# Kernel optimization log

Hardware: AMD Instinct MI355X
Metric: run time of the kernel (lower is better)

The kernel has to match this reference:

```python
import jax, jax.numpy as jnp
import numpy as np

B, N, IN_DIM, OUT_DIM, H = 8, 1024, 256, 256, 4
HD = OUT_DIM // H  # head_dim = 64
NEG = -1e9
EPS = 1e-5


def setup_inputs() -> dict:
    key = jax.random.key(0)
    ks = jax.random.split(key, 9)
    h = jax.random.normal(ks[0], (B, N, IN_DIM), dtype=jnp.float32)
    adj = jax.random.randint(ks[1], (N, N), 0, 2, dtype=jnp.int32)
    adj = adj.at[jnp.arange(N), jnp.arange(N)].set(1)  # self loops so no empty rows
    s = 1.0 / np.sqrt(IN_DIM)
    W = jax.random.uniform(ks[2], (H, IN_DIM, HD), jnp.float32, -s, s)
    sa = 1.0 / np.sqrt(2 * HD)
    a1 = jax.random.uniform(ks[3], (H, HD), jnp.float32, -sa, sa)
    a2 = jax.random.uniform(ks[4], (H, HD), jnp.float32, -sa, sa)
    sp = 1.0 / np.sqrt(OUT_DIM)
    proj_w = jax.random.uniform(ks[5], (OUT_DIM, OUT_DIM), jnp.float32, -sp, sp)
    proj_b = jax.random.uniform(ks[6], (OUT_DIM,), jnp.float32, -sp, sp)
    gamma = jnp.ones((OUT_DIM,), jnp.float32)
    beta = jnp.zeros((OUT_DIM,), jnp.float32)
    return {"h": h, "adj": adj, "W": W, "a1": a1, "a2": a2,
            "proj_w": proj_w, "proj_b": proj_b, "gamma": gamma, "beta": beta}


def reference(h, adj, W, a1, a2, proj_w, proj_b, gamma, beta):
    # Wh: [B,H,N,HD]
    Wh = jnp.einsum('bni,hid->bhnd', h, W)
    # Decompose a([Wh_i || Wh_j]) = a1.Wh_i + a2.Wh_j (same math as concat+linear)
    si = jnp.einsum('bhnd,hd->bhn', Wh, a1)  # [B,H,N]
    sj = jnp.einsum('bhnd,hd->bhn', Wh, a2)
    e = jax.nn.leaky_relu(si[:, :, :, None] + sj[:, :, None, :], 0.2)  # [B,H,N,N]
    mask = (adj == 0)  # [N,N]
    e = jnp.where(mask[None, None], NEG, e)
    alpha = jax.nn.softmax(e, axis=-1)
    out = jnp.einsum('bhnm,bhmd->bhnd', alpha, Wh)  # [B,H,N,HD]
    h_multi = out.transpose(0, 2, 1, 3).reshape(B, N, OUT_DIM)  # concat heads
    h_out = jnp.einsum('bnd,od->bno', h_multi, proj_w) + proj_b
    h_out = h_out + h  # residual (in_dim == out_dim)
    mu = jnp.mean(h_out, axis=-1, keepdims=True)
    var = jnp.mean(jnp.square(h_out - mu), axis=-1, keepdims=True)
    return (h_out - mu) * jax.lax.rsqrt(var + EPS) * gamma + beta
```

## Files before the change

### kernel.cpp

```cpp
#include <hip/hip_runtime.h>
#include <hip/hip_bf16.h>

#define BB 8
#define NN 1024
#define IN_DIM 256
#define OUT_DIM 256
#define NH 4
#define HD 64
#define TN 16
#define PSTRIDE 1032

typedef __attribute__((ext_vector_type(8))) short short8;
typedef __attribute__((ext_vector_type(4))) short short4e;
typedef __attribute__((ext_vector_type(4))) float floatx4;
typedef __attribute__((ext_vector_type(4))) int intx4;

__global__ __launch_bounds__(256) void prep_kernel(
    const float* __restrict__ W,
    const float* __restrict__ a1, const float* __restrict__ a2,
    const float* __restrict__ proj_w,
    __hip_bfloat16* __restrict__ WTb,
    __hip_bfloat16* __restrict__ pwb,
    __hip_bfloat16* __restrict__ wab)
{
    int blk = blockIdx.x, t = threadIdx.x;
    if (blk < 16) {
        int o = blk * 16 + (t >> 4);
        int hh = o >> 6, d = o & 63;
        #pragma unroll
        for (int kk = 0; kk < 16; ++kk) {
            int k = (t & 15) + 16 * kk;
            WTb[(size_t)o * 256 + k] = __float2bfloat16(W[((size_t)hh * 256 + k) * 64 + d]);
        }
    } else if (blk < 32) {
        size_t base = (size_t)(blk - 16) * 4096 + t * 16;
        #pragma unroll
        for (int k = 0; k < 16; k += 4) {
            floatx4 v = *(const floatx4*)(proj_w + base + k);
            alignas(8) __hip_bfloat16 tmp[4];
            #pragma unroll
            for (int j = 0; j < 4; ++j) tmp[j] = __float2bfloat16(v[j]);
            *(short4e*)(pwb + base + k) = *(const short4e*)tmp;
        }
    } else {
        int r = blk - 32;
        int hh = r & 3;
        const float* av = (r < 4 ? a1 : a2) + hh * HD;
        const float* wrow = W + ((size_t)hh * 256 + t) * HD;
        float s = 0.f;
        #pragma unroll 8
        for (int d = 0; d < HD; ++d) s += wrow[d] * av[d];
        wab[(size_t)r * 256 + t] = __float2bfloat16(s);
        wab[(size_t)(r + 8) * 256 + t] = __float2bfloat16(0.f);
    }
}

__global__ __launch_bounds__(256) void wh_mfma_kernel(
    const float* __restrict__ h,
    const __hip_bfloat16* __restrict__ WTb,
    const __hip_bfloat16* __restrict__ wab,
    __hip_bfloat16* __restrict__ WhT,
    float* __restrict__ si, float* __restrict__ sj)
{
    int t = threadIdx.x;
    int w = t >> 6, l = t & 63;
    int rl = l & 15, q = l >> 4;
    int r0 = blockIdx.x * 16;

    short8 af[8];
    const float* Arow = h + (size_t)(r0 + rl) * 256 + q * 8;
    #pragma unroll
    for (int k0 = 0; k0 < 8; ++k0) {
        floatx4 v0 = *(const floatx4*)(Arow + k0 * 32);
        floatx4 v1 = *(const floatx4*)(Arow + k0 * 32 + 4);
        short8 a;
        #pragma unroll
        for (int j = 0; j < 4; ++j) {
            a[j]     = (short)(__bfloat16_as_ushort(__float2bfloat16(v0[j])));
            a[j + 4] = (short)(__bfloat16_as_ushort(__float2bfloat16(v1[j])));
        }
        af[k0] = a;
    }

    int bb = r0 >> 10;
    int n0 = (r0 & 1023) + q * 4;

    #pragma unroll
    for (int j = 0; j < 4; ++j) {
        int ct = w + j * 4;
        const __hip_bfloat16* Brow = WTb + (size_t)(ct * 16 + rl) * 256 + q * 8;
        floatx4 acc = {0.f, 0.f, 0.f, 0.f};
        #pragma unroll
        for (int k0 = 0; k0 < 8; ++k0) {
            short8 bf = *(const short8*)(Brow + k0 * 32);
            acc = __builtin_amdgcn_mfma_f32_16x16x32_bf16(af[k0], bf, acc, 0, 0, 0);
        }
        int o = ct * 16 + rl;
        int hh = o >> 6, d = o & 63;
        alignas(8) __hip_bfloat16 tmp[4];
        #pragma unroll
        for (int i = 0; i < 4; ++i) tmp[i] = __float2bfloat16(acc[i]);
        *(short4e*)(WhT + ((size_t)(bb * NH + hh) * HD + d) * NN + n0) = *(const short4e*)tmp;
    }

    if (w == 0) {
        const __hip_bfloat16* Brow = wab + (size_t)rl * 256 + q * 8;
        floatx4 acc = {0.f, 0.f, 0.f, 0.f};
        #pragma unroll
        for (int k0 = 0; k0 < 8; ++k0) {
            short8 bf = *(const short8*)(Brow + k0 * 32);
            acc = __builtin_amdgcn_mfma_f32_16x16x32_bf16(af[k0], bf, acc, 0, 0, 0);
        }
        if (rl < 8) {
            int hh = rl & 3;
            float* dst = (rl < 4 ? si : sj) + ((size_t)(bb * NH + hh)) * NN + n0;
            *(floatx4*)dst = acc;
        }
    }
}

__global__ __launch_bounds__(256) void attn_kernel(
    const int* __restrict__ adj,
    const __hip_bfloat16* __restrict__ WhT,
    const float* __restrict__ si,
    const float* __restrict__ sj,
    __hip_bfloat16* __restrict__ hmb)
{
    int bx = blockIdx.x;
    int bh = bx >> 6;
    int n0 = (bx & 63) * TN;
    int t = threadIdx.x;

    __shared__ __align__(16) __hip_bfloat16 p_lds[TN * PSTRIDE];
    __shared__ float rinv[TN];

    int r = t >> 4;
    int c = t & 15;
    int n = n0 + r;
    float sii = si[(size_t)bh * NN + n];
    const float* sjr = sj + (size_t)bh * NN;
    const int* adjr = adj + (size_t)n * NN;

    float lsum = 0.f;
    #pragma unroll 4
    for (int jj = 0; jj < 16; ++jj) {
        int m = jj * 64 + c * 4;
        floatx4 s4 = *(const floatx4*)(sjr + m);
        intx4 a4 = *(const intx4*)(adjr + m);
        alignas(8) __hip_bfloat16 tmp[4];
        #pragma unroll
        for (int k = 0; k < 4; ++k) {
            float x = sii + s4[k];
            x = x > 0.f ? x : 0.2f * x;
            x = (a4[k] == 0) ? -1e9f : x;
            float pv = __expf(x);
            lsum += pv;
            tmp[k] = __float2bfloat16(pv);
        }
        *(short4e*)(p_lds + (size_t)r * PSTRIDE + m) = *(const short4e*)tmp;
    }
    #pragma unroll
    for (int off = 1; off < 16; off <<= 1) lsum += __shfl_xor(lsum, off, 64);
    if (c == 0) rinv[r] = 1.f / lsum;
    __syncthreads();

    int w = t >> 6;
    int l = t & 63;
    int rl = l & 15, q = l >> 4;
    int d0 = w * 16;
    const __hip_bfloat16* Bbase = WhT + ((size_t)bh * HD + d0 + rl) * NN + q * 8;
    const __hip_bfloat16* Abase = p_lds + (size_t)rl * PSTRIDE + q * 8;

    floatx4 acc = {0.f, 0.f, 0.f, 0.f};
    #pragma unroll 4
    for (int k0 = 0; k0 < NN; k0 += 32) {
        short8 af = *(const short8*)(Abase + k0);
        short8 bf = *(const short8*)(Bbase + k0);
        acc = __builtin_amdgcn_mfma_f32_16x16x32_bf16(af, bf, acc, 0, 0, 0);
    }

    int b = bh >> 2, hhh = bh & 3;
    #pragma unroll
    for (int i = 0; i < 4; ++i) {
        int nr = q * 4 + i;
        float v = acc[i] * rinv[nr];
        hmb[((size_t)(b * NN) + n0 + nr) * OUT_DIM + hhh * HD + d0 + rl] = __float2bfloat16(v);
    }
}

__global__ __launch_bounds__(256) void proj_ln_kernel(
    const __hip_bfloat16* __restrict__ hmb,
    const float* __restrict__ h,
    const __hip_bfloat16* __restrict__ pwb,
    const float* __restrict__ proj_b,
    const float* __restrict__ gamma,
    const float* __restrict__ beta,
    float* __restrict__ out)
{
    int t = threadIdx.x;
    int w = t >> 6, l = t & 63;
    int rl = l & 15, q = l >> 4;
    int r0 = blockIdx.x * 16;

    __shared__ float red[2][4][16];

    short8 af[8];
    const __hip_bfloat16* Arow = hmb + (size_t)(r0 + rl) * 256 + q * 8;
    #pragma unroll
    for (int k0 = 0; k0 < 8; ++k0) af[k0] = *(const short8*)(Arow + k0 * 32);

    floatx4 acc[4];
    #pragma unroll
    for (int j = 0; j < 4; ++j) {
        int ct = w + j * 4;
        const __hip_bfloat16* Brow = pwb + (size_t)(ct * 16 + rl) * 256 + q * 8;
        floatx4 a = {0.f, 0.f, 0.f, 0.f};
        #pragma unroll
        for (int k0 = 0; k0 < 8; ++k0) {
            short8 bf = *(const short8*)(Brow + k0 * 32);
            a = __builtin_amdgcn_mfma_f32_16x16x32_bf16(af[k0], bf, a, 0, 0, 0);
        }
        acc[j] = a;
    }

    float ps[4] = {0.f, 0.f, 0.f, 0.f};
    #pragma unroll
    for (int j = 0; j < 4; ++j) {
        int col = (w + j * 4) * 16 + rl;
        float pb = proj_b[col];
        #pragma unroll
        for (int i = 0; i < 4; ++i) {
            float v = acc[j][i] + pb + h[(size_t)(r0 + q * 4 + i) * 256 + col];
            acc[j][i] = v;
            ps[i] += v;
        }
    }
    #pragma unroll
    for (int i = 0; i < 4; ++i) {
        float s = ps[i];
        #pragma unroll
        for (int off = 1; off < 16; off <<= 1) s += __shfl_xor(s, off, 64);
        ps[i] = s;
    }
    if (rl == 0) {
        for (int i = 0; i < 4; ++i) red[0][w][q * 4 + i] = ps[i];
    }
    __syncthreads();
    float mu[4];
    #pragma unroll
    for (int i = 0; i < 4; ++i) {
        int row = q * 4 + i;
        mu[i] = (red[0][0][row] + red[0][1][row] + red[0][2][row] + red[0][3][row]) * (1.f / 256.f);
    }

    float vs[4] = {0.f, 0.f, 0.f, 0.f};
    #pragma unroll
    for (int j = 0; j < 4; ++j) {
        #pragma unroll
        for (int i = 0; i < 4; ++i) { float cv = acc[j][i] - mu[i]; vs[i] += cv * cv; }
    }
    #pragma unroll
    for (int i = 0; i < 4; ++i) {
        float s = vs[i];
        #pragma unroll
        for (int off = 1; off < 16; off <<= 1) s += __shfl_xor(s, off, 64);
        vs[i] = s;
    }
    if (rl == 0) {
        for (int i = 0; i < 4; ++i) red[1][w][q * 4 + i] = vs[i];
    }
    __syncthreads();
    float rs[4];
    #pragma unroll
    for (int i = 0; i < 4; ++i) {
        int row = q * 4 + i;
        float var = (red[1][0][row] + red[1][1][row] + red[1][2][row] + red[1][3][row]) * (1.f / 256.f);
        rs[i] = rsqrtf(var + 1e-5f);
    }

    #pragma unroll
    for (int j = 0; j < 4; ++j) {
        int col = (w + j * 4) * 16 + rl;
        float g = gamma[col], be = beta[col];
        #pragma unroll
        for (int i = 0; i < 4; ++i)
            out[(size_t)(r0 + q * 4 + i) * 256 + col] = (acc[j][i] - mu[i]) * rs[i] * g + be;
    }
}

extern "C" void kernel_launch(void* const* d_in, const int* in_sizes, int n_in,
                              void* d_out, int out_size, void* d_ws, size_t ws_size,
                              hipStream_t stream) {
    const float* h      = (const float*)d_in[0];
    const int*   adj    = (const int*)d_in[1];
    const float* W      = (const float*)d_in[2];
    const float* a1     = (const float*)d_in[3];
    const float* a2     = (const float*)d_in[4];
    const float* proj_w = (const float*)d_in[5];
    const float* proj_b = (const float*)d_in[6];
    const float* gamma  = (const float*)d_in[7];
    const float* beta   = (const float*)d_in[8];
    float* out = (float*)d_out;

    char* ws = (char*)d_ws;
    __hip_bfloat16* WhT = (__hip_bfloat16*)ws;                    ws += (size_t)BB*NH*HD*NN*2;
    __hip_bfloat16* hmb = (__hip_bfloat16*)ws;                    ws += (size_t)BB*NN*OUT_DIM*2;
    __hip_bfloat16* WTb = (__hip_bfloat16*)ws;                    ws += 256*256*2;
    __hip_bfloat16* pwb = (__hip_bfloat16*)ws;                    ws += 256*256*2;
    __hip_bfloat16* wab = (__hip_bfloat16*)ws;                    ws += 16*256*2;
    float* si = (float*)ws;                                       ws += (size_t)BB*NH*NN*4;
    float* sj = (float*)ws;

    prep_kernel<<<40, 256, 0, stream>>>(W, a1, a2, proj_w, WTb, pwb, wab);
    wh_mfma_kernel<<<512, 256, 0, stream>>>(h, WTb, wab, WhT, si, sj);
    attn_kernel<<<BB * NH * (NN / TN), 256, 0, stream>>>(adj, WhT, si, sj, hmb);
    proj_ln_kernel<<<512, 256, 0, stream>>>(hmb, h, pwb, proj_b, gamma, beta, out);
}
```

Before: 144.7 us.

## Fuse all four GAT stages into one cooperative kernel with grid syncs

Replaces the four separate launches (prep, Wh GEMM, attention, projection+LayerNorm) with a single cooperative kernel of 512 blocks that separates the stages with grid-wide syncs. Each block processes four attention tiles in a loop. The aim is to remove launch overhead and inter-kernel gaps. In exchange it adds grid barrier cost, and occupancy is limited because every block now reserves the attention stage's ~33KB LDS buffer even during the GEMM phases. The cooperative launch also needs all 512 blocks to be co-resident.

```diff
diff --git a/kernel.cpp b/kernel.cpp
--- a/kernel.cpp
+++ b/kernel.cpp
@@ -1,5 +1,8 @@
 #include <hip/hip_runtime.h>
 #include <hip/hip_bf16.h>
+#include <hip/hip_cooperative_groups.h>
+
+namespace cg = cooperative_groups;
 
 #define BB 8
 #define NN 1024
@@ -15,15 +18,28 @@
 typedef __attribute__((ext_vector_type(4))) float floatx4;
 typedef __attribute__((ext_vector_type(4))) int intx4;
 
-__global__ __launch_bounds__(256) void prep_kernel(
-    const float* __restrict__ W,
-    const float* __restrict__ a1, const float* __restrict__ a2,
-    const float* __restrict__ proj_w,
+__global__ __launch_bounds__(256) void fused_gat_kernel(
+    const float* __restrict__ h, const int* __restrict__ adj,
+    const float* __restrict__ W, const float* __restrict__ a1, const float* __restrict__ a2,
+    const float* __restrict__ proj_w, const float* __restrict__ proj_b,
+    const float* __restrict__ gamma, const float* __restrict__ beta,
+    float* __restrict__ out,
     __hip_bfloat16* __restrict__ WTb,
     __hip_bfloat16* __restrict__ pwb,
-    __hip_bfloat16* __restrict__ wab)
+    __hip_bfloat16* __restrict__ wab,
+    __hip_bfloat16* __restrict__ WhT,
+    float* __restrict__ si, float* __restrict__ sj,
+    __hip_bfloat16* __restrict__ hmb)
 {
+    cg::grid_group grid = cg::this_grid();
     int blk = blockIdx.x, t = threadIdx.x;
+    int w = t >> 6, l = t & 63;
+    int rl = l & 15, q = l >> 4;
+
+    __shared__ __align__(16) __hip_bfloat16 p_lds[TN * PSTRIDE];
+    __shared__ float rinv[TN];
+    __shared__ float red[2][4][16];
+
     if (blk < 16) {
         int o = blk * 16 + (t >> 4);
         int hh = o >> 6, d = o & 63;
@@ -42,7 +58,7 @@
             for (int j = 0; j < 4; ++j) tmp[j] = __float2bfloat16(v[j]);
             *(short4e*)(pwb + base + k) = *(const short4e*)tmp;
         }
-    } else {
+    } else if (blk < 40) {
         int r = blk - 32;
         int hh = r & 3;
         const float* av = (r < 4 ? a1 : a2) + hh * HD;
@@ -53,238 +69,209 @@
         wab[(size_t)r * 256 + t] = __float2bfloat16(s);
         wab[(size_t)(r + 8) * 256 + t] = __float2bfloat16(0.f);
     }
-}
-
-__global__ __launch_bounds__(256) void wh_mfma_kernel(
-    const float* __restrict__ h,
-    const __hip_bfloat16* __restrict__ WTb,
-    const __hip_bfloat16* __restrict__ wab,
-    __hip_bfloat16* __restrict__ WhT,
-    float* __restrict__ si, float* __restrict__ sj)
-{
-    int t = threadIdx.x;
-    int w = t >> 6, l = t & 63;
-    int rl = l & 15, q = l >> 4;
-    int r0 = blockIdx.x * 16;
-
-    short8 af[8];
-    const float* Arow = h + (size_t)(r0 + rl) * 256 + q * 8;
-    #pragma unroll
-    for (int k0 = 0; k0 < 8; ++k0) {
-        floatx4 v0 = *(const floatx4*)(Arow + k0 * 32);
-        floatx4 v1 = *(const floatx4*)(Arow + k0 * 32 + 4);
-        short8 a;
-        #pragma unroll
-        for (int j = 0; j < 4; ++j) {
-            a[j]     = (short)(__bfloat16_as_ushort(__float2bfloat16(v0[j])));
-            a[j + 4] = (short)(__bfloat16_as_ushort(__float2bfloat16(v1[j])));
-        }
-        af[k0] = a;
+    __threadfence();
+    grid.sync();
+
+    {
+        int r0 = blk * 16;
+        short8 af[8];
+        const float* Arow = h + (size_t)(r0 + rl) * 256 + q * 8;
+        #pragma unroll
+        for (int k0 = 0; k0 < 8; ++k0) {
+            floatx4 v0 = *(const floatx4*)(Arow + k0 * 32);
+            floatx4 v1 = *(const floatx4*)(Arow + k0 * 32 + 4);
+            short8 a;
+            #pragma unroll
+            for (int j = 0; j < 4; ++j) {
+                a[j]     = (short)(__bfloat16_as_ushort(__float2bfloat16(v0[j])));
+                a[j + 4] = (short)(__bfloat16_as_ushort(__float2bfloat16(v1[j])));
+            }
+            af[k0] = a;
+        }
+
+        int bb = r0 >> 10;
+        int n0 = (r0 & 1023) + q * 4;
+
+        #pragma unroll
+        for (int j = 0; j < 4; ++j) {
+            int ct = w + j * 4;
+            const __hip_bfloat16* Brow = WTb + (size_t)(ct * 16 + rl) * 256 + q * 8;
+            floatx4 acc = {0.f, 0.f, 0.f, 0.f};
+            #pragma unroll
+            for (int k0 = 0; k0 < 8; ++k0) {
+                short8 bf = *(const short8*)(Brow + k0 * 32);
+                acc = __builtin_amdgcn_mfma_f32_16x16x32_bf16(af[k0], bf, acc, 0, 0, 0);
+            }
+            int o = ct * 16 + rl;
+            int hh = o >> 6, d = o & 63;
+            alignas(8) __hip_bfloat16 tmp[4];
+            #pragma unroll
+            for (int i = 0; i < 4; ++i) tmp[i] = __float2bfloat16(acc[i]);
+            *(short4e*)(WhT + ((size_t)(bb * NH + hh) * HD + d) * NN + n0) = *(const short4e*)tmp;
+        }
+
+        if (w == 0) {
+            const __hip_bfloat16* Brow = wab + (size_t)rl * 256 + q * 8;
+            floatx4 acc = {0.f, 0.f, 0.f, 0.f};
+            #pragma unroll
+            for (int k0 = 0; k0 < 8; ++k0) {
+                short8 bf = *(const short8*)(Brow + k0 * 32);
+                acc = __builtin_amdgcn_mfma_f32_16x16x32_bf16(af[k0], bf, acc, 0, 0, 0);
+            }
+            if (rl < 8) {
+                int hh = rl & 3;
+                float* dst = (rl < 4 ? si : sj) + ((size_t)(bb * NH + hh)) * NN + n0;
+                *(floatx4*)dst = acc;
+            }
+        }
     }
-
-    int bb = r0 >> 10;
-    int n0 = (r0 & 1023) + q * 4;
-
-    #pragma unroll
-    for (int j = 0; j < 4; ++j) {
-        int ct = w + j * 4;
-        const __hip_bfloat16* Brow = WTb + (size_t)(ct * 16 + rl) * 256 + q * 8;
+    __threadfence();
+    grid.sync();
+
+    for (int it = 0; it < 4; ++it) {
+        __syncthreads();
+        int bx = blk * 4 + it;
+        int bh = bx >> 6;
+        int n0 = (bx & 63) * TN;
+
+        int r = t >> 4;
+        int c = t & 15;
+        int n = n0 + r;
+        float sii = si[(size_t)bh * NN + n];
+        const float* sjr = sj + (size_t)bh * NN;
+        const int* adjr = adj + (size_t)n * NN;
+
+        float lsum = 0.f;
+        #pragma unroll 4
+        for (int jj = 0; jj < 16; ++jj) {
+            int m = jj * 64 + c * 4;
+            floatx4 s4 = *(const floatx4*)(sjr + m);
+            intx4 a4 = *(const intx4*)(adjr + m);
+            alignas(8) __hip_bfloat16 tmp[4];
+            #pragma unroll
+            for (int k = 0; k < 4; ++k) {
+                float x = sii + s4[k];
+                x = x > 0.f ? x : 0.2f * x;
+                x = (a4[k] == 0) ? -1e9f : x;
+                float pv = __expf(x);
+                lsum += pv;
+                tmp[k] = __float2bfloat16(pv);
+            }
+            *(short4e*)(p_lds + (size_t)r * PSTRIDE + m) = *(const short4e*)tmp;
+        }
+        #pragma unroll
+        for (int off = 1; off < 16; off <<= 1) lsum += __shfl_xor(lsum, off, 64);
+        if (c == 0) rinv[r] = 1.f / lsum;
+        __syncthreads();
+
+        int d0 = w * 16;
+        const __hip_bfloat16* Bbase = WhT + ((size_t)bh * HD + d0 + rl) * NN + q * 8;
+        const __hip_bfloat16* Abase = p_lds + (size_t)rl * PSTRIDE + q * 8;
+
         floatx4 acc = {0.f, 0.f, 0.f, 0.f};
-        #pragma unroll
-        for (int k0 = 0; k0 < 8; ++k0) {
-            short8 bf = *(const short8*)(Brow + k0 * 32);
-            acc = __builtin_amdgcn_mfma_f32_16x16x32_bf16(af[k0], bf, acc, 0, 0, 0);
-        }
-        int o = ct * 16 + rl;
-        int hh = o >> 6, d = o & 63;
-        alignas(8) __hip_bfloat16 tmp[4];
-        #pragma unroll
-        for (int i = 0; i < 4; ++i) tmp[i] = __float2bfloat16(acc[i]);
-        *(short4e*)(WhT + ((size_t)(bb * NH + hh) * HD + d) * NN + n0) = *(const short4e*)tmp;
+        #pragma unroll 4
+        for (int k0 = 0; k0 < NN; k0 += 32) {
+            short8 af = *(const short8*)(Abase + k0);
+            short8 bf = *(const short8*)(Bbase + k0);
+            acc = __builtin_amdgcn_mfma_f32_16x16x32_bf16(af, bf, acc, 0, 0, 0);
+        }
+
+        int b = bh >> 2, hhh = bh & 3;
+        #pragma unroll
+        for (int i = 0; i < 4; ++i) {
+            int nr = q * 4 + i;
+            float v = acc[i] * rinv[nr];
+            hmb[((size_t)(b * NN) + n0 + nr) * OUT_DIM + hhh * HD + d0 + rl] = __float2bfloat16(v);
+        }
     }
-
-    if (w == 0) {
-        const __hip_bfloat16* Brow = wab + (size_t)rl * 256 + q * 8;
-        floatx4 acc = {0.f, 0.f, 0.f, 0.f};
-        #pragma unroll
-        for (int k0 = 0; k0 < 8; ++k0) {
-            short8 bf = *(const short8*)(Brow + k0 * 32);
-            acc = __builtin_amdgcn_mfma_f32_16x16x32_bf16(af[k0], bf, acc, 0, 0, 0);
-        }
-        if (rl < 8) {
-            int hh = rl & 3;
-            float* dst = (rl < 4 ? si : sj) + ((size_t)(bb * NH + hh)) * NN + n0;
-            *(floatx4*)dst = acc;
-        }
-    }
-}
-
-__global__ __launch_bounds__(256) void attn_kernel(
-    const int* __restrict__ adj,
-    const __hip_bfloat16* __restrict__ WhT,
-    const float* __restrict__ si,
-    const float* __restrict__ sj,
-    __hip_bfloat16* __restrict__ hmb)
-{
-    int bx = blockIdx.x;
-    int bh = bx >> 6;
-    int n0 = (bx & 63) * TN;
-    int t = threadIdx.x;
-
-    __shared__ __align__(16) __hip_bfloat16 p_lds[TN * PSTRIDE];
-    __shared__ float rinv[TN];
-
-    int r = t >> 4;
-    int c = t & 15;
-    int n = n0 + r;
-    float sii = si[(size_t)bh * NN + n];
-    const float* sjr = sj + (size_t)bh * NN;
-    const int* adjr = adj + (size_t)n * NN;
-
-    float lsum = 0.f;
-    #pragma unroll 4
-    for (int jj = 0; jj < 16; ++jj) {
-        int m = jj * 64 + c * 4;
-        floatx4 s4 = *(const floatx4*)(sjr + m);
-        intx4 a4 = *(const intx4*)(adjr + m);
-        alignas(8) __hip_bfloat16 tmp[4];
-        #pragma unroll
-        for (int k = 0; k < 4; ++k) {
-            float x = sii + s4[k];
-            x = x > 0.f ? x : 0.2f * x;
-            x = (a4[k] == 0) ? -1e9f : x;
-            float pv = __expf(x);
-            lsum += pv;
-            tmp[k] = __float2bfloat16(pv);
-        }
-        *(short4e*)(p_lds + (size_t)r * PSTRIDE + m) = *(const short4e*)tmp;
-    }
-    #pragma unroll
-    for (int off = 1; off < 16; off <<= 1) lsum += __shfl_xor(lsum, off, 64);
-    if (c == 0) rinv[r] = 1.f / lsum;
-    __syncthreads();
-
-    int w = t >> 6;
-    int l = t & 63;
-    int rl = l & 15, q = l >> 4;
-    int d0 = w * 16;
-    const __hip_bfloat16* Bbase = WhT + ((size_t)bh * HD + d0 + rl) * NN + q * 8;
-    const __hip_bfloat16* Abase = p_lds + (size_t)rl * PSTRIDE + q * 8;
-
-    floatx4 acc = {0.f, 0.f, 0.f, 0.f};
-    #pragma unroll 4
-    for (int k0 = 0; k0 < NN; k0 += 32) {
-        short8 af = *(const short8*)(Abase + k0);
-        short8 bf = *(const short8*)(Bbase + k0);
-        acc = __builtin_amdgcn_mfma_f32_16x16x32_bf16(af, bf, acc, 0, 0, 0);
-    }
-
-    int b = bh >> 2, hhh = bh & 3;
-    #pragma unroll
-    for (int i = 0; i < 4; ++i) {
-        int nr = q * 4 + i;
-        float v = acc[i] * rinv[nr];
-        hmb[((size_t)(b * NN) + n0 + nr) * OUT_DIM + hhh * HD + d0 + rl] = __float2bfloat16(v);
-    }
-}
-
-__global__ __launch_bounds__(256) void proj_ln_kernel(
-    const __hip_bfloat16* __restrict__ hmb,
-    const float* __restrict__ h,
-    const __hip_bfloat16* __restrict__ pwb,
-    const float* __restrict__ proj_b,
-    const float* __restrict__ gamma,
-    const float* __restrict__ beta,
-    float* __restrict__ out)
-{
-    int t = threadIdx.x;
-    int w = t >> 6, l = t & 63;
-    int rl = l & 15, q = l >> 4;
-    int r0 = blockIdx.x * 16;
-
-    __shared__ float red[2][4][16];
-
-    short8 af[8];
-    const __hip_bfloat16* Arow = hmb + (size_t)(r0 + rl) * 256 + q * 8;
-    #pragma unroll
-    for (int k0 = 0; k0 < 8; ++k0) af[k0] = *(const short8*)(Arow + k0 * 32);
-
-    floatx4 acc[4];
-    #pragma unroll
-    for (int j = 0; j < 4; ++j) {
-        int ct = w + j * 4;
-        const __hip_bfloat16* Brow = pwb + (size_t)(ct * 16 + rl) * 256 + q * 8;
-        floatx4 a = {0.f, 0.f, 0.f, 0.f};
-        #pragma unroll
-        for (int k0 = 0; k0 < 8; ++k0) {
-            short8 bf = *(const short8*)(Brow + k0 * 32);
-            a = __builtin_amdgcn_mfma_f32_16x16x32_bf16(af[k0], bf, a, 0, 0, 0);
-        }
-        acc[j] = a;
-    }
-
-    float ps[4] = {0.f, 0.f, 0.f, 0.f};
-    #pragma unroll
-    for (int j = 0; j < 4; ++j) {
-        int col = (w + j * 4) * 16 + rl;
-        float pb = proj_b[col];
-        #pragma unroll
-        for (int i = 0; i < 4; ++i) {
-            float v = acc[j][i] + pb + h[(size_t)(r0 + q * 4 + i) * 256 + col];
-            acc[j][i] = v;
-            ps[i] += v;
-        }
-    }
-    #pragma unroll
-    for (int i = 0; i < 4; ++i) {
-        float s = ps[i];
-        #pragma unroll
-        for (int off = 1; off < 16; off <<= 1) s += __shfl_xor(s, off, 64);
-        ps[i] = s;
-    }
-    if (rl == 0) {
-        for (int i = 0; i < 4; ++i) red[0][w][q * 4 + i] = ps[i];
-    }
-    __syncthreads();
-    float mu[4];
-    #pragma unroll
-    for (int i = 0; i < 4; ++i) {
-        int row = q * 4 + i;
-        mu[i] = (red[0][0][row] + red[0][1][row] + red[0][2][row] + red[0][3][row]) * (1.f / 256.f);
-    }
-
-    float vs[4] = {0.f, 0.f, 0.f, 0.f};
-    #pragma unroll
-    for (int j = 0; j < 4; ++j) {
-        #pragma unroll
-        for (int i = 0; i < 4; ++i) { float cv = acc[j][i] - mu[i]; vs[i] += cv * cv; }
-    }
-    #pragma unroll
-    for (int i = 0; i < 4; ++i) {
-        float s = vs[i];
-        #pragma unroll
-        for (int off = 1; off < 16; off <<= 1) s += __shfl_xor(s, off, 64);
-        vs[i] = s;
-    }
-    if (rl == 0) {
-        for (int i = 0; i < 4; ++i) red[1][w][q * 4 + i] = vs[i];
-    }
-    __syncthreads();
-    float rs[4];
-    #pragma unroll
-    for (int i = 0; i < 4; ++i) {
-        int row = q * 4 + i;
-        float var = (red[1][0][row] + red[1][1][row] + red[1][2][row] + red[1][3][row]) * (1.f / 256.f);
-        rs[i] = rsqrtf(var + 1e-5f);
-    }
-
-    #pragma unroll
-    for (int j = 0; j < 4; ++j) {
-        int col = (w + j * 4) * 16 + rl;
-        float g = gamma[col], be = beta[col];
-        #pragma unroll
-        for (int i = 0; i < 4; ++i)
-            out[(size_t)(r0 + q * 4 + i) * 256 + col] = (acc[j][i] - mu[i]) * rs[i] * g + be;
+    __threadfence();
+    grid.sync();
+
+    {
+        int r0 = blk * 16;
+        short8 af[8];
+        const __hip_bfloat16* Arow = hmb + (size_t)(r0 + rl) * 256 + q * 8;
+        #pragma unroll
+        for (int k0 = 0; k0 < 8; ++k0) af[k0] = *(const short8*)(Arow + k0 * 32);
+
+        floatx4 acc[4];
+        #pragma unroll
+        for (int j = 0; j < 4; ++j) {
+            int ct = w + j * 4;
+            const __hip_bfloat16* Brow = pwb + (size_t)(ct * 16 + rl) * 256 + q * 8;
+            floatx4 a = {0.f, 0.f, 0.f, 0.f};
+            #pragma unroll
+            for (int k0 = 0; k0 < 8; ++k0) {
+                short8 bf = *(const short8*)(Brow + k0 * 32);
+                a = __builtin_amdgcn_mfma_f32_16x16x32_bf16(af[k0], bf, a, 0, 0, 0);
+            }
+            acc[j] = a;
+        }
+
+        float ps[4] = {0.f, 0.f, 0.f, 0.f};
+        #pragma unroll
+        for (int j = 0; j < 4; ++j) {
+            int col = (w + j * 4) * 16 + rl;
+            float pb = proj_b[col];
+            #pragma unroll
+            for (int i = 0; i < 4; ++i) {
+                float v = acc[j][i] + pb + h[(size_t)(r0 + q * 4 + i) * 256 + col];
+                acc[j][i] = v;
+                ps[i] += v;
+            }
+        }
+        #pragma unroll
+        for (int i = 0; i < 4; ++i) {
+            float s = ps[i];
+            #pragma unroll
+            for (int off = 1; off < 16; off <<= 1) s += __shfl_xor(s, off, 64);
+            ps[i] = s;
+        }
+        __syncthreads();
+        if (rl == 0) {
+            for (int i = 0; i < 4; ++i) red[0][w][q * 4 + i] = ps[i];
+        }
+        __syncthreads();
+        float mu[4];
+        #pragma unroll
+        for (int i = 0; i < 4; ++i) {
+            int row = q * 4 + i;
+            mu[i] = (red[0][0][row] + red[0][1][row] + red[0][2][row] + red[0][3][row]) * (1.f / 256.f);
+        }
+
+        float vs[4] = {0.f, 0.f, 0.f, 0.f};
+        #pragma unroll
+        for (int j = 0; j < 4; ++j) {
+            #pragma unroll
+            for (int i = 0; i < 4; ++i) { float cv = acc[j][i] - mu[i]; vs[i] += cv * cv; }
+        }
+        #pragma unroll
+        for (int i = 0; i < 4; ++i) {
+            float s = vs[i];
+            #pragma unroll
+            for (int off = 1; off < 16; off <<= 1) s += __shfl_xor(s, off, 64);
+            vs[i] = s;
+        }
+        if (rl == 0) {
+            for (int i = 0; i < 4; ++i) red[1][w][q * 4 + i] = vs[i];
+        }
+        __syncthreads();
+        float rs[4];
+        #pragma unroll
+        for (int i = 0; i < 4; ++i) {
+            int row = q * 4 + i;
+            float var = (red[1][0][row] + red[1][1][row] + red[1][2][row] + red[1][3][row]) * (1.f / 256.f);
+            rs[i] = rsqrtf(var + 1e-5f);
+        }
+
+        #pragma unroll
+        for (int j = 0; j < 4; ++j) {
+            int col = (w + j * 4) * 16 + rl;
+            float g = gamma[col], be = beta[col];
+            #pragma unroll
+            for (int i = 0; i < 4; ++i)
+                out[(size_t)(r0 + q * 4 + i) * 256 + col] = (acc[j][i] - mu[i]) * rs[i] * g + be;
+        }
     }
 }
 
@@ -311,8 +298,9 @@
     float* si = (float*)ws;                                       ws += (size_t)BB*NH*NN*4;
     float* sj = (float*)ws;
 
-    prep_kernel<<<40, 256, 0, stream>>>(W, a1, a2, proj_w, WTb, pwb, wab);
-    wh_mfma_kernel<<<512, 256, 0, stream>>>(h, WTb, wab, WhT, si, sj);
-    attn_kernel<<<BB * NH * (NN / TN), 256, 0, stream>>>(adj, WhT, si, sj, hmb);
-    proj_ln_kernel<<<512, 256, 0, stream>>>(hmb, h, pwb, proj_b, gamma, beta, out);
+    void* args[] = { (void*)&h, (void*)&adj, (void*)&W, (void*)&a1, (void*)&a2,
+                     (void*)&proj_w, (void*)&proj_b, (void*)&gamma, (void*)&beta,
+                     (void*)&out, (void*)&WTb, (void*)&pwb, (void*)&wab,
+                     (void*)&WhT, (void*)&si, (void*)&sj, (void*)&hmb };
+    hipLaunchCooperativeKernel((void*)fused_gat_kernel, dim3(512), dim3(256), args, 0, stream);
 }
```

Result: slower. 455.9 us (+215.0%).

## Bit-pack adjacency mask and tile attention softmax-PV over key chunks

Applied to the files above, without the earlier changes.

Adds a prep stage that packs the int32 adjacency matrix into 32-bit bitmasks, so the attention kernel reads 128 KB of mask instead of 4 MB repeated across all batch-head blocks. The attention kernel now builds probabilities in 128-key chunks, each followed by its MFMA accumulation, which shrinks LDS use from about 33 KB to about 4 KB per block and allows more resident blocks. The cost is two barriers per chunk, plus extra prep work and workspace for the mask.

```diff
diff --git a/kernel.cpp b/kernel.cpp
--- a/kernel.cpp
+++ b/kernel.cpp
@@ -8,7 +8,8 @@
 #define NH 4
 #define HD 64
 #define TN 16
-#define PSTRIDE 1032
+#define TM 128
+#define PSTR 136
 
 typedef __attribute__((ext_vector_type(8))) short short8;
 typedef __attribute__((ext_vector_type(4))) short short4e;
@@ -18,10 +19,11 @@
 __global__ __launch_bounds__(256) void prep_kernel(
     const float* __restrict__ W,
     const float* __restrict__ a1, const float* __restrict__ a2,
-    const float* __restrict__ proj_w,
+    const float* __restrict__ proj_w, const int* __restrict__ adj,
     __hip_bfloat16* __restrict__ WTb,
     __hip_bfloat16* __restrict__ pwb,
-    __hip_bfloat16* __restrict__ wab)
+    __hip_bfloat16* __restrict__ wab,
+    unsigned* __restrict__ adjm)
 {
     int blk = blockIdx.x, t = threadIdx.x;
     if (blk < 16) {
@@ -42,7 +44,7 @@
             for (int j = 0; j < 4; ++j) tmp[j] = __float2bfloat16(v[j]);
             *(short4e*)(pwb + base + k) = *(const short4e*)tmp;
         }
-    } else {
+    } else if (blk < 40) {
         int r = blk - 32;
         int hh = r & 3;
         const float* av = (r < 4 ? a1 : a2) + hh * HD;
@@ -52,6 +54,19 @@
         for (int d = 0; d < HD; ++d) s += wrow[d] * av[d];
         wab[(size_t)r * 256 + t] = __float2bfloat16(s);
         wab[(size_t)(r + 8) * 256 + t] = __float2bfloat16(0.f);
+    } else {
+        int bp = blk - 40;
+        int n = bp * 8 + (t >> 5);
+        int wd = t & 31;
+        const int* arow = adj + (size_t)n * NN + wd * 32;
+        unsigned bits = 0;
+        #pragma unroll
+        for (int j4 = 0; j4 < 8; ++j4) {
+            intx4 v = *(const intx4*)(arow + j4 * 4);
+            #pragma unroll
+            for (int j = 0; j < 4; ++j) if (v[j] != 0) bits |= (1u << (j4 * 4 + j));
+        }
+        adjm[(size_t)n * 32 + wd] = bits;
     }
 }
 
@@ -120,7 +135,7 @@
 }
 
 __global__ __launch_bounds__(256) void attn_kernel(
-    const int* __restrict__ adj,
+    const unsigned* __restrict__ adjm,
     const __hip_bfloat16* __restrict__ WhT,
     const float* __restrict__ si,
     const float* __restrict__ sj,
@@ -131,53 +146,54 @@
     int n0 = (bx & 63) * TN;
     int t = threadIdx.x;
 
-    __shared__ __align__(16) __hip_bfloat16 p_lds[TN * PSTRIDE];
+    __shared__ __align__(16) __hip_bfloat16 p_lds[TN * PSTR];
     __shared__ float rinv[TN];
 
-    int r = t >> 4;
-    int c = t & 15;
+    int r = t >> 4, c = t & 15;
     int n = n0 + r;
     float sii = si[(size_t)bh * NN + n];
     const float* sjr = sj + (size_t)bh * NN;
-    const int* adjr = adj + (size_t)n * NN;
+    const unsigned* amrow = adjm + (size_t)n * 32;
+
+    int w = t >> 6, l = t & 63;
+    int rl = l & 15, q = l >> 4;
+    int d0 = w * 16;
+    const __hip_bfloat16* Bb = WhT + ((size_t)bh * HD + d0 + rl) * NN + q * 8;
+    const __hip_bfloat16* Ab = p_lds + (size_t)rl * PSTR + q * 8;
 
     float lsum = 0.f;
-    #pragma unroll 4
-    for (int jj = 0; jj < 16; ++jj) {
-        int m = jj * 64 + c * 4;
-        floatx4 s4 = *(const floatx4*)(sjr + m);
-        intx4 a4 = *(const intx4*)(adjr + m);
-        alignas(8) __hip_bfloat16 tmp[4];
-        #pragma unroll
-        for (int k = 0; k < 4; ++k) {
-            float x = sii + s4[k];
+    floatx4 acc = {0.f, 0.f, 0.f, 0.f};
+
+    for (int m0 = 0; m0 < NN; m0 += TM) {
+        floatx4 s0 = *(const floatx4*)(sjr + m0 + c * 8);
+        floatx4 s1 = *(const floatx4*)(sjr + m0 + c * 8 + 4);
+        unsigned wv = amrow[(m0 >> 5) + (c >> 2)];
+        unsigned sh = (c & 3) * 8;
+        alignas(16) __hip_bfloat16 tmp[8];
+        #pragma unroll
+        for (int k = 0; k < 8; ++k) {
+            float x = sii + (k < 4 ? s0[k] : s1[k - 4]);
             x = x > 0.f ? x : 0.2f * x;
-            x = (a4[k] == 0) ? -1e9f : x;
+            x = ((wv >> (sh + k)) & 1u) ? x : -1e9f;
             float pv = __expf(x);
             lsum += pv;
             tmp[k] = __float2bfloat16(pv);
         }
-        *(short4e*)(p_lds + (size_t)r * PSTRIDE + m) = *(const short4e*)tmp;
-    }
+        *(short8*)(p_lds + (size_t)r * PSTR + c * 8) = *(const short8*)tmp;
+        __syncthreads();
+        #pragma unroll
+        for (int ks = 0; ks < 4; ++ks) {
+            short8 af = *(const short8*)(Ab + ks * 32);
+            short8 bf = *(const short8*)(Bb + m0 + ks * 32);
+            acc = __builtin_amdgcn_mfma_f32_16x16x32_bf16(af, bf, acc, 0, 0, 0);
+        }
+        __syncthreads();
+    }
+
     #pragma unroll
     for (int off = 1; off < 16; off <<= 1) lsum += __shfl_xor(lsum, off, 64);
     if (c == 0) rinv[r] = 1.f / lsum;
     __syncthreads();
-
-    int w = t >> 6;
-    int l = t & 63;
-    int rl = l & 15, q = l >> 4;
-    int d0 = w * 16;
-    const __hip_bfloat16* Bbase = WhT + ((size_t)bh * HD + d0 + rl) * NN + q * 8;
-    const __hip_bfloat16* Abase = p_lds + (size_t)rl * PSTRIDE + q * 8;
-
-    floatx4 acc = {0.f, 0.f, 0.f, 0.f};
-    #pragma unroll 4
-    for (int k0 = 0; k0 < NN; k0 += 32) {
-        short8 af = *(const short8*)(Abase + k0);
-        short8 bf = *(const short8*)(Bbase + k0);
-        acc = __builtin_amdgcn_mfma_f32_16x16x32_bf16(af, bf, acc, 0, 0, 0);
-    }
 
     int b = bh >> 2, hhh = bh & 3;
     #pragma unroll
@@ -309,10 +325,11 @@
     __hip_bfloat16* pwb = (__hip_bfloat16*)ws;                    ws += 256*256*2;
     __hip_bfloat16* wab = (__hip_bfloat16*)ws;                    ws += 16*256*2;
     float* si = (float*)ws;                                       ws += (size_t)BB*NH*NN*4;
-    float* sj = (float*)ws;
-
-    prep_kernel<<<40, 256, 0, stream>>>(W, a1, a2, proj_w, WTb, pwb, wab);
+    float* sj = (float*)ws;                                       ws += (size_t)BB*NH*NN*4;
+    unsigned* adjm = (unsigned*)ws;                               ws += (size_t)NN*32*4;
+
+    prep_kernel<<<168, 256, 0, stream>>>(W, a1, a2, proj_w, adj, WTb, pwb, wab, adjm);
     wh_mfma_kernel<<<512, 256, 0, stream>>>(h, WTb, wab, WhT, si, sj);
-    attn_kernel<<<BB * NH * (NN / TN), 256, 0, stream>>>(adj, WhT, si, sj, hmb);
+    attn_kernel<<<BB * NH * (NN / TN), 256, 0, stream>>>(adjm, WhT, si, sj, hmb);
     proj_ln_kernel<<<512, 256, 0, stream>>>(hmb, h, pwb, proj_b, gamma, beta, out);
 }
```

Result: no change. 142.0 us (-1.9%).
